# Kernel optimization log

Hardware: AMD Instinct MI355X
Metric: run time of the kernel (lower is better)

## Reference

```python
import jax, jax.numpy as jnp
import numpy as np

N = 500000          # number of points
KS = 9              # kernel_size -> k = KS*KS = 81 neighbors
K = KS * KS
C = 4               # xyz (3) + dist (1)
OUT = 8             # out_channels


def setup_inputs() -> dict:
    key = jax.random.key(0)
    k1, k2, k3, k4, k5 = jax.random.split(key, 5)
    points = jax.random.normal(k1, (N, 3), dtype=jnp.float32)
    indices = jax.random.randint(k2, (N, K), 0, N, dtype=jnp.int64)
    # make first neighbor self (loop=True in knn_graph)
    indices = indices.at[:, 0].set(jnp.arange(N, dtype=jnp.int64))
    dw = jax.random.normal(k3, (K, C), dtype=jnp.float32)
    weight = jax.random.normal(k4, (C, K, OUT), dtype=jnp.float32)
    bias = jax.random.normal(k5, (OUT,), dtype=jnp.float32)
    return {"points": points, "indices": indices, "dw": dw,
            "weight": weight, "bias": bias}


def reference(points, indices, dw, weight, bias):
    # gather neighbor coordinates: [N, K, 3]
    selected = points[indices]
    # squared distance to the first (self) neighbor, +1: [N, K]
    dist = jnp.sum((selected - selected[:, :1]) ** 2, axis=-1) + 1.0
    # concat coords with dist feature: [N, K, C]
    data = jnp.concatenate((selected, dist[..., None]), axis=-1)
    # per-(neighbor, channel) elementwise weight
    data = dw * data
    # contract neighbors and channels into output: [N, OUT]
    out = jnp.einsum('njc,cjl->nl', data, weight) + bias
    return out
```

## Files before the change

kernel.cpp:

```cpp
#include <hip/hip_runtime.h>
#include <hip/hip_fp16.h>

#define K_NB 81
#define OUTC 8
#define BLK 256
#define KT 16

typedef float v2f __attribute__((ext_vector_type(2)));

__global__ void prep_w2(const float* __restrict__ dw,
                        const float* __restrict__ wt,
                        float* __restrict__ w2) {
    int i = blockIdx.x * blockDim.x + threadIdx.x;
    if (i < K_NB * 32) {
        int k = i >> 5;
        int c = (i >> 3) & 3;
        int l = i & 7;
        w2[i] = dw[k * 4 + c] * wt[(c * K_NB + k) * OUTC + l];
    }
}

union F2H { float f; __half2 h; };

__global__ void repack_points(const float* __restrict__ pts,
                              v2f* __restrict__ ph, int N) {
    int n = blockIdx.x * blockDim.x + threadIdx.x;
    if (n >= N) return;
    float x = pts[3 * n + 0], y = pts[3 * n + 1], z = pts[3 * n + 2];
    F2H a, b;
    a.h = __floats2half2_rn(x, y);
    b.h = __floats2half2_rn(z, 0.f);
    v2f v; v.x = a.f; v.y = b.f;
    ph[n] = v;
}

__global__ __launch_bounds__(BLK) void conv_main_h(
    const float* __restrict__ points,
    const v2f*   __restrict__ ph,
    const int*   __restrict__ indices,
    const float* __restrict__ w2,
    const float* __restrict__ bias,
    float*       __restrict__ out,
    int N) {
    __shared__ int sidx[BLK * (KT + 1)];

    const int tid = threadIdx.x;
    const int n0  = blockIdx.x * BLK;
    const int n   = n0 + tid;
    const bool valid = n < N;
    const int nc = valid ? n : (N - 1);

    const float px = points[nc * 3 + 0];
    const float py = points[nc * 3 + 1];
    const float pz = points[nc * 3 + 2];

    float acc[OUTC];
#pragma unroll
    for (int l = 0; l < OUTC; ++l) {
        float a = bias[l] + w2[24 + l];
        a = fmaf(px, w2[0 + l], a);
        a = fmaf(py, w2[8 + l], a);
        a = fmaf(pz, w2[16 + l], a);
        acc[l] = a;
    }

    for (int t = 0; t < 5; ++t) {
        __syncthreads();
#pragma unroll
        for (int i = 0; i < KT; ++i) {
            int e   = i * BLK + tid;
            int row = e >> 4;
            int col = e & 15;
            int gr  = n0 + row;
            if (gr >= N) gr = N - 1;
            sidx[row * (KT + 1) + col] =
                __builtin_nontemporal_load(&indices[gr * K_NB + 1 + t * KT + col]);
        }
        __syncthreads();

        int ids[KT];
#pragma unroll
        for (int j = 0; j < KT; ++j)
            ids[j] = sidx[tid * (KT + 1) + j];

        v2f r[KT];
#pragma unroll
        for (int j = 0; j < KT; ++j) {
            const v2f* ap = ph + ids[j];
            asm volatile("global_load_dwordx2 %0, %1, off sc0"
                         : "=v"(r[j]) : "v"(ap));
        }
        asm volatile("s_waitcnt vmcnt(0)" ::: "memory");
        __builtin_amdgcn_sched_barrier(0);

#pragma unroll
        for (int j = 0; j < KT; ++j) {
            const int k = 1 + t * KT + j;
            F2H u0, u1; u0.f = r[j].x; u1.f = r[j].y;
            const float2 fxy = __half22float2(u0.h);
            const float  qx = fxy.x, qy = fxy.y;
            const float  qz = __half2float(__low2half(u1.h));
            const float dx = qx - px, dy = qy - py, dz = qz - pz;
            const float dist = fmaf(dx, dx, fmaf(dy, dy, fmaf(dz, dz, 1.0f)));
            const float* __restrict__ w = w2 + k * 32;
#pragma unroll
            for (int l = 0; l < OUTC; ++l) {
                acc[l] = fmaf(qx, w[l],
                         fmaf(qy, w[8 + l],
                         fmaf(qz, w[16 + l],
                         fmaf(dist, w[24 + l], acc[l]))));
            }
        }
    }

    if (valid) {
        float4* o = (float4*)(out + (long)n * OUTC);
        o[0] = make_float4(acc[0], acc[1], acc[2], acc[3]);
        o[1] = make_float4(acc[4], acc[5], acc[6], acc[7]);
    }
}

__global__ __launch_bounds__(BLK) void conv_main_f32(
    const float* __restrict__ points,
    const int*   __restrict__ indices,
    const float* __restrict__ w2,
    const float* __restrict__ bias,
    float*       __restrict__ out,
    int N) {
    __shared__ int sidx[BLK * (KT + 1)];
    const int tid = threadIdx.x;
    const int n0  = blockIdx.x * BLK;
    const int n   = n0 + tid;
    const bool valid = n < N;
    const int nc = valid ? n : (N - 1);

    const float px = points[nc * 3 + 0];
    const float py = points[nc * 3 + 1];
    const float pz = points[nc * 3 + 2];
    float acc[OUTC];
#pragma unroll
    for (int l = 0; l < OUTC; ++l) {
        float a = bias[l] + w2[24 + l];
        a = fmaf(px, w2[0 + l], a);
        a = fmaf(py, w2[8 + l], a);
        a = fmaf(pz, w2[16 + l], a);
        acc[l] = a;
    }
    for (int t = 0; t < 5; ++t) {
        __syncthreads();
#pragma unroll
        for (int i = 0; i < KT; ++i) {
            int e = i * BLK + tid;
            int row = e >> 4, col = e & 15;
            int gr = n0 + row;
            if (gr >= N) gr = N - 1;
            sidx[row * (KT + 1) + col] = indices[gr * K_NB + 1 + t * KT + col];
        }
        __syncthreads();
#pragma unroll
        for (int j = 0; j < KT; ++j) {
            const int k  = 1 + t * KT + j;
            const int id = sidx[tid * (KT + 1) + j];
            const float qx = points[id * 3 + 0];
            const float qy = points[id * 3 + 1];
            const float qz = points[id * 3 + 2];
            const float dx = qx - px, dy = qy - py, dz = qz - pz;
            const float dist = fmaf(dx, dx, fmaf(dy, dy, fmaf(dz, dz, 1.0f)));
            const float* __restrict__ w = w2 + k * 32;
#pragma unroll
            for (int l = 0; l < OUTC; ++l) {
                acc[l] = fmaf(qx, w[l],
                         fmaf(qy, w[8 + l],
                         fmaf(qz, w[16 + l],
                         fmaf(dist, w[24 + l], acc[l]))));
            }
        }
    }
    if (valid) {
        float4* o = (float4*)(out + (long)n * OUTC);
        o[0] = make_float4(acc[0], acc[1], acc[2], acc[3]);
        o[1] = make_float4(acc[4], acc[5], acc[6], acc[7]);
    }
}

extern "C" void kernel_launch(void* const* d_in, const int* in_sizes, int n_in,
                              void* d_out, int out_size, void* d_ws, size_t ws_size,
                              hipStream_t stream) {
    const float* points  = (const float*)d_in[0];
    const int*   indices = (const int*)  d_in[1];
    const float* dw      = (const float*)d_in[2];
    const float* wt      = (const float*)d_in[3];
    const float* bias    = (const float*)d_in[4];
    float*       out     = (float*)d_out;

    const int N = in_sizes[0] / 3;

    const size_t ph_bytes = (size_t)N * 8;
    const size_t need     = ph_bytes + K_NB * 32 * sizeof(float);

    if (ws_size >= need) {
        v2f*   ph = (v2f*)d_ws;
        float* w2 = (float*)((char*)d_ws + ph_bytes);
        hipLaunchKernelGGL(prep_w2, dim3((K_NB * 32 + BLK - 1) / BLK), dim3(BLK),
                           0, stream, dw, wt, w2);
        hipLaunchKernelGGL(repack_points, dim3((N + BLK - 1) / BLK), dim3(BLK),
                           0, stream, points, ph, N);
        hipLaunchKernelGGL(conv_main_h, dim3((N + BLK - 1) / BLK), dim3(BLK),
                           0, stream, points, ph, indices, w2, bias, out, N);
    } else {
        float* w2 = (float*)d_ws;
        hipLaunchKernelGGL(prep_w2, dim3((K_NB * 32 + BLK - 1) / BLK), dim3(BLK),
                           0, stream, dw, wt, w2);
        hipLaunchKernelGGL(conv_main_f32, dim3((N + BLK - 1) / BLK), dim3(BLK),
                           0, stream, points, indices, w2, bias, out, N);
    }
}
```

Measured before the change: 434.4 us.

## Software-pipeline index loads and neighbor gathers with double-buffered shared indices

Restructures the main half-precision kernel so that the index tile for step t+2 and the point gathers for step t+1 are issued before the FMA work for step t runs. It uses a two-slot shared-memory index buffer, a register double buffer for gathered points, and manual vmcnt waits. The aim is to hide the latency of the random gathers and index loads behind compute, and to drop one barrier per step. In exchange it raises VGPR pressure, which may lower occupancy. Reusing a shared slot with only one barrier per step also leaves a possible write-after-read race between waves.

After: 441.1 us. Within noise of the previous version (+1.5%).

```diff
diff --git a/kernel.cpp b/kernel.cpp
--- a/kernel.cpp
+++ b/kernel.cpp
@@ -5,6 +5,7 @@
 #define OUTC 8
 #define BLK 256
 #define KT 16
+#define NT 5
 
 typedef float v2f __attribute__((ext_vector_type(2)));
 
@@ -42,7 +43,7 @@
     const float* __restrict__ bias,
     float*       __restrict__ out,
     int N) {
-    __shared__ int sidx[BLK * (KT + 1)];
+    __shared__ int sidx[2][BLK * (KT + 1)];
 
     const int tid = threadIdx.x;
     const int n0  = blockIdx.x * BLK;
@@ -64,39 +65,90 @@
         acc[l] = a;
     }
 
-    for (int t = 0; t < 5; ++t) {
-        __syncthreads();
-#pragma unroll
-        for (int i = 0; i < KT; ++i) {
-            int e   = i * BLK + tid;
-            int row = e >> 4;
-            int col = e & 15;
-            int gr  = n0 + row;
-            if (gr >= N) gr = N - 1;
-            sidx[row * (KT + 1) + col] =
-                __builtin_nontemporal_load(&indices[gr * K_NB + 1 + t * KT + col]);
-        }
-        __syncthreads();
-
-        int ids[KT];
-#pragma unroll
-        for (int j = 0; j < KT; ++j)
-            ids[j] = sidx[tid * (KT + 1) + j];
-
-        v2f r[KT];
-#pragma unroll
-        for (int j = 0; j < KT; ++j) {
-            const v2f* ap = ph + ids[j];
-            asm volatile("global_load_dwordx2 %0, %1, off sc0"
-                         : "=v"(r[j]) : "v"(ap));
-        }
-        asm volatile("s_waitcnt vmcnt(0)" ::: "memory");
+    unsigned vb[KT];
+#pragma unroll
+    for (int i = 0; i < KT; ++i) {
+        int e = i * BLK + tid;
+        int row = e >> 4, col = e & 15;
+        int gr = n0 + row;
+        if (gr >= N) gr = N - 1;
+        vb[i] = (unsigned)(gr * K_NB + 1 + col) * 4u;
+    }
+
+    int sv[KT];
+    int ids[KT];
+    v2f r[2][KT];
+
+#pragma unroll
+    for (int i = 0; i < KT; ++i)
+        asm volatile("global_load_dword %0, %1, %2 nt"
+                     : "=&v"(sv[i]) : "v"(vb[i]), "s"(indices));
+    asm volatile("s_waitcnt vmcnt(0)" ::: "memory");
+    __builtin_amdgcn_sched_barrier(0);
+#pragma unroll
+    for (int i = 0; i < KT; ++i) {
+        int e = i * BLK + tid;
+        int row = e >> 4, col = e & 15;
+        sidx[0][row * (KT + 1) + col] = sv[i];
+    }
+    __syncthreads();
+#pragma unroll
+    for (int j = 0; j < KT; ++j) ids[j] = sidx[0][tid * (KT + 1) + j];
+#pragma unroll
+    for (int j = 0; j < KT; ++j) {
+        unsigned off = (unsigned)ids[j] * 8u;
+        asm volatile("global_load_dwordx2 %0, %1, %2 sc0"
+                     : "=&v"(r[0][j]) : "v"(off), "s"(ph));
+    }
+#pragma unroll
+    for (int i = 0; i < KT; ++i)
+        asm volatile("global_load_dword %0, %1, %2 nt"
+                     : "=&v"(sv[i]) : "v"(vb[i] + 64u), "s"(indices));
+
+#pragma unroll
+    for (int t = 0; t < NT; ++t) {
+        if (t < NT - 1) {
+            asm volatile("s_waitcnt vmcnt(16)" ::: "memory");
+        } else {
+            asm volatile("s_waitcnt vmcnt(0)" ::: "memory");
+        }
         __builtin_amdgcn_sched_barrier(0);
+
+        if (t < NT - 1) {
+            asm volatile("s_waitcnt vmcnt(0)" ::: "memory");
+            __builtin_amdgcn_sched_barrier(0);
+#pragma unroll
+            for (int i = 0; i < KT; ++i) {
+                int e = i * BLK + tid;
+                int row = e >> 4, col = e & 15;
+                sidx[(t + 1) & 1][row * (KT + 1) + col] = sv[i];
+            }
+            __syncthreads();
+
+#pragma unroll
+            for (int j = 0; j < KT; ++j)
+                ids[j] = sidx[(t + 1) & 1][tid * (KT + 1) + j];
+#pragma unroll
+            for (int j = 0; j < KT; ++j) {
+                unsigned off = (unsigned)ids[j] * 8u;
+                asm volatile("global_load_dwordx2 %0, %1, %2 sc0"
+                             : "=&v"(r[(t + 1) & 1][j]) : "v"(off), "s"(ph));
+            }
+            if (t < NT - 2) {
+#pragma unroll
+                for (int i = 0; i < KT; ++i)
+                    asm volatile("global_load_dword %0, %1, %2 nt"
+                                 : "=&v"(sv[i])
+                                 : "v"(vb[i] + 64u * (unsigned)(t + 2)),
+                                   "s"(indices));
+            }
+            __builtin_amdgcn_sched_barrier(0);
+        }
 
 #pragma unroll
         for (int j = 0; j < KT; ++j) {
             const int k = 1 + t * KT + j;
-            F2H u0, u1; u0.f = r[j].x; u1.f = r[j].y;
+            F2H u0, u1; u0.f = r[t & 1][j].x; u1.f = r[t & 1][j].y;
             const float2 fxy = __half22float2(u0.h);
             const float  qx = fxy.x, qy = fxy.y;
             const float  qz = __half2float(__low2half(u1.h));
@@ -146,7 +198,7 @@
         a = fmaf(pz, w2[16 + l], a);
         acc[l] = a;
     }
-    for (int t = 0; t < 5; ++t) {
+    for (int t = 0; t < NT; ++t) {
         __syncthreads();
 #pragma unroll
         for (int i = 0; i < KT; ++i) {
```
